# Kernel optimization log

Hardware: AMD Instinct MI355X
Metric: run time of the kernel (lower is better)

## Reference

```python
import jax, jax.numpy as jnp
import numpy as np

DATA_MAX = 30.0
LOG_FACTOR = float(np.log(DATA_MAX + 1.0))
THRESHOLDS = np.array([0.1, 1.0, 2.0, 5.0, 8.0], dtype=np.float32)
HIGHS = np.array([1.0, 2.0, 5.0, 8.0, np.inf], dtype=np.float32)
LEVEL_WEIGHTS = np.array([0.1, 0.1, 0.2, 0.25, 0.35], dtype=np.float32)
TIME_WEIGHTS = np.array([0.0075, 0.02, 0.03, 0.04, 0.05, 0.06, 0.07, 0.08, 0.09, 0.1,
                         0.09, 0.08, 0.07, 0.06, 0.05, 0.04, 0.03, 0.02, 0.0075, 0.005],
                        dtype=np.float32)


def setup_inputs() -> dict:
    key = jax.random.key(0)
    k1, k2, k3 = jax.random.split(key, 3)
    shape = (2, 20, 480, 480)
    pred_norm = jax.random.uniform(k1, shape, dtype=jnp.float32)
    target_norm = jax.random.uniform(k2, shape, dtype=jnp.float32)
    mask = jax.random.uniform(k3, shape, dtype=jnp.float32)
    return {"pred_norm": pred_norm, "target_norm": target_norm, "mask": mask}


def _metscore(pred_norm, target_norm, mask):
    # de-normalize to physical space (mm)
    pred = jnp.clip(jnp.expm1(pred_norm * LOG_FACTOR), 0.0, None)
    target = jnp.clip(jnp.expm1(target_norm * LOG_FACTOR), 0.0, None)
    B, T, H, W = pred.shape
    N = B * H * W
    # flatten each timestep across batch+space: [T, N]
    p = jnp.transpose(pred, (1, 0, 2, 3)).reshape(T, N)
    t = jnp.transpose(target, (1, 0, 2, 3)).reshape(T, N)
    m = (jnp.transpose(mask, (1, 0, 2, 3)).reshape(T, N) > 0.5)
    mf = m.astype(p.dtype)

    thr = jnp.asarray(THRESHOLDS)
    highs = jnp.asarray(HIGHS)
    lw = jnp.asarray(LEVEL_WEIGHTS)

    # ---- per-timestep masked correlation (excluding double-zero pixels) ----
    dz = (p < thr[0]) & (t < thr[0])
    mc = (m & ~dz).astype(p.dtype)                       # [T,N]
    cnt = mc.sum(-1)                                      # [T]
    safe_cnt = jnp.maximum(cnt, 1.0)
    p_mean = (p * mc).sum(-1) / safe_cnt
    t_mean = (t * mc).sum(-1) / safe_cnt
    dp = (p - p_mean[:, None]) * mc
    dt = (t - t_mean[:, None]) * mc
    num = (dp * dt).sum(-1)
    den = jnp.sqrt((dp * dp).sum(-1) * (dt * dt).sum(-1))
    r_time = jnp.where(cnt > 0, jnp.clip(num / (den + 1e-6), -1.0, 1.0), 0.0)  # [T]

    # ---- threshold-bin membership [T, L, N] ----
    p_in = ((p[:, None, :] >= thr[None, :, None]) & (p[:, None, :] < highs[None, :, None])).astype(p.dtype)
    t_in = ((t[:, None, :] >= thr[None, :, None]) & (t[:, None, :] < highs[None, :, None])).astype(p.dtype)

    hits = jnp.einsum('tln,tln,tn->tl', p_in, t_in, mf)   # [T,L]
    p_tot = jnp.einsum('tln,tn->tl', p_in, mf)            # hits + false alarms
    t_tot = jnp.einsum('tln,tn->tl', t_in, mf)            # hits + misses
    ts_mat = hits / (p_tot + t_tot - hits + 1e-8)         # [T,L]

    diff = jnp.abs(p - t) * mf                            # [T,N]
    mae_num = jnp.einsum('tln,tn->tl', t_in, diff)
    mae_mat = jnp.where(t_tot > 0, mae_num / jnp.maximum(t_tot, 1.0), 0.0)  # [T,L]

    # ---- score combination ----
    term_corr = jnp.sqrt(jnp.exp(r_time - 1.0))           # [T]
    term_mae = jnp.sqrt(jnp.exp(-mae_mat / 100.0))        # [T,L]
    score_time = term_corr * (lw[None, :] * ts_mat * term_mae).sum(-1)  # [T]

    tw = jnp.asarray(TIME_WEIGHTS)
    if T == tw.shape[0]:
        w_time = tw
    elif T < tw.shape[0]:
        w_time = tw[:T] / tw[:T].sum()
    else:
        w_time = jnp.ones((T,), dtype=p.dtype) / T
    total = (score_time * w_time).sum()
    return total, score_time, r_time, ts_mat, mae_mat, ts_mat.mean(0), mae_mat.mean(0)


def reference(pred_norm, target_norm, mask):
    return _metscore(pred_norm, target_norm, mask)
```

## Files before the change

kernel.cpp:

```cpp
#include <hip/hip_runtime.h>
#include <math.h>

#define TS   20
#define NL   5
#define NS   26
#define HW4C 57600

__device__ __forceinline__ void accum_pixel(float pn, float tn, float mn, float* a)
{
    constexpr float LF = 3.4339872044851463f;
    float p = fmaxf(expf(pn * LF) - 1.0f, 0.0f);
    float q = fmaxf(expf(tn * LF) - 1.0f, 0.0f);
    if (mn > 0.5f) {
        if (!((p < 0.1f) && (q < 0.1f))) {
            a[20] += 1.0f;
            a[21] += p;  a[22] += q;
            a[23] += p * q;  a[24] += p * p;  a[25] += q * q;
        }
        float ad = fabsf(p - q);
        bool p1 = p >= 0.1f, p2 = p >= 1.0f, p3 = p >= 2.0f, p4 = p >= 5.0f, p5 = p >= 8.0f;
        bool q1 = q >= 0.1f, q2 = q >= 1.0f, q3 = q >= 2.0f, q4 = q >= 5.0f, q5 = q >= 8.0f;
        bool pin[NL] = { p1 && !p2, p2 && !p3, p3 && !p4, p4 && !p5, p5 };
        bool qin[NL] = { q1 && !q2, q2 && !q3, q3 && !q4, q4 && !q5, q5 };
        #pragma unroll
        for (int l = 0; l < NL; ++l) {
            if (pin[l])           a[5 + l]  += 1.0f;
            if (qin[l])         { a[10 + l] += 1.0f;  a[15 + l] += ad; }
            if (pin[l] && qin[l]) a[l]      += 1.0f;
        }
    }
}

__global__ __launch_bounds__(256) void metscore_pass1(
    const float4* __restrict__ pred, const float4* __restrict__ targ,
    const float4* __restrict__ mask, float* __restrict__ sums )
{
    const int t = blockIdx.y;
    const int b = blockIdx.z;
    const size_t base = ((size_t)b * TS + t) * (size_t)HW4C;

    float acc[NS];
    #pragma unroll
    for (int k = 0; k < NS; ++k) acc[k] = 0.0f;

    const int stride = gridDim.x * blockDim.x;
    for (int i = blockIdx.x * blockDim.x + threadIdx.x; i < HW4C; i += stride) {
        float4 pv = pred[base + i];
        float4 tv = targ[base + i];
        float4 mv = mask[base + i];
        accum_pixel(pv.x, tv.x, mv.x, acc);
        accum_pixel(pv.y, tv.y, mv.y, acc);
        accum_pixel(pv.z, tv.z, mv.z, acc);
        accum_pixel(pv.w, tv.w, mv.w, acc);
    }

    #pragma unroll
    for (int k = 0; k < NS; ++k) {
        float v = acc[k];
        v += __shfl_down(v, 32);
        v += __shfl_down(v, 16);
        v += __shfl_down(v, 8);
        v += __shfl_down(v, 4);
        v += __shfl_down(v, 2);
        v += __shfl_down(v, 1);
        acc[k] = v;
    }

    __shared__ float lds[4][NS];
    const int lane = threadIdx.x & 63;
    const int wv   = threadIdx.x >> 6;
    if (lane == 0) {
        #pragma unroll
        for (int k = 0; k < NS; ++k) lds[wv][k] = acc[k];
    }
    __syncthreads();
    if (threadIdx.x < NS) {
        float s = lds[0][threadIdx.x] + lds[1][threadIdx.x]
                + lds[2][threadIdx.x] + lds[3][threadIdx.x];
        atomicAdd(&sums[t * NS + threadIdx.x], s);
    }
}

__global__ __launch_bounds__(128) void metscore_final(
    const float* __restrict__ sums, float* __restrict__ out)
{
    __shared__ float ts_s[TS][NL];
    __shared__ float mae_s[TS][NL];
    __shared__ float sc_s[TS];

    const int tid = threadIdx.x;

    if (tid < TS * NL) {
        int t = tid / NL, l = tid % NL;
        const float* s = sums + t * NS;
        float h = s[l], pt = s[5 + l], tt = s[10 + l], mn = s[15 + l];
        float ts  = h / (pt + tt - h + 1e-8f);
        float mae = (tt > 0.0f) ? (mn / fmaxf(tt, 1.0f)) : 0.0f;
        ts_s[t][l]  = ts;
        mae_s[t][l] = mae;
        out[41 + tid]  = ts;
        out[141 + tid] = mae;
    }
    __syncthreads();

    if (tid < TS) {
        const float* s = sums + tid * NS;
        double cnt = s[20], sp = s[21], st = s[22];
        double spt = s[23], spp = s[24], stt = s[25];
        double sc = fmax(cnt, 1.0);
        double pm = sp / sc, tm = st / sc;
        double num = spt - pm * st - tm * sp + pm * tm * cnt;
        double vp  = spp - 2.0 * pm * sp + pm * pm * cnt;
        double vt  = stt - 2.0 * tm * st + tm * tm * cnt;
        double den = sqrt(vp * vt);
        double r = num / (den + 1e-6);
        r = fmin(fmax(r, -1.0), 1.0);
        float rt = (cnt > 0.0) ? (float)r : 0.0f;
        out[21 + tid] = rt;

        const float LW[NL] = {0.1f, 0.1f, 0.2f, 0.25f, 0.35f};
        float term_corr = sqrtf(expf(rt - 1.0f));
        float accl = 0.0f;
        #pragma unroll
        for (int l = 0; l < NL; ++l)
            accl += LW[l] * ts_s[tid][l] * sqrtf(expf(-mae_s[tid][l] * 0.01f));
        float sct = term_corr * accl;
        out[1 + tid] = sct;

        const float TW[TS] = {0.0075f, 0.02f, 0.03f, 0.04f, 0.05f, 0.06f, 0.07f,
                              0.08f, 0.09f, 0.1f, 0.09f, 0.08f, 0.07f, 0.06f,
                              0.05f, 0.04f, 0.03f, 0.02f, 0.0075f, 0.005f};
        sc_s[tid] = sct * TW[tid];
    }
    __syncthreads();

    if (tid == 0) {
        float tot = 0.0f;
        for (int t = 0; t < TS; ++t) tot += sc_s[t];
        out[0] = tot;
    }
    if (tid < NL) {
        float a = 0.0f, b = 0.0f;
        for (int t = 0; t < TS; ++t) { a += ts_s[t][tid]; b += mae_s[t][tid]; }
        out[241 + tid] = a * (1.0f / TS);
        out[246 + tid] = b * (1.0f / TS);
    }
}

extern "C" void kernel_launch(void* const* d_in, const int* in_sizes, int n_in,
                              void* d_out, int out_size, void* d_ws, size_t ws_size,
                              hipStream_t stream) {
    (void)in_sizes; (void)n_in; (void)out_size; (void)ws_size;
    const float4* pred = (const float4*)d_in[0];
    const float4* targ = (const float4*)d_in[1];
    const float4* mask = (const float4*)d_in[2];
    float* out  = (float*)d_out;
    float* sums = (float*)d_ws;

    hipMemsetAsync(sums, 0, TS * NS * sizeof(float), stream);

    dim3 grid(32, TS, 2);
    metscore_pass1<<<grid, 256, 0, stream>>>(pred, targ, mask, sums);
    metscore_final<<<1, 128, 0, stream>>>(sums, out);
}
```

Before: 144.8 us.

## Fuse final reduction via last-block counter and pack bin counts into integers

Replaces per-bin float accumulators with 5-bit packed integer one-hot counters, cumulative MAE sums differenced at the end, and branchless masking with fast exp. Each block processes a fixed unrolled tile, and the grid is resized to cover the data exactly. The separate finalization kernel is folded into the main kernel using an atomic completion counter so the last block computes the scores. This reduces ALU and branch work per pixel and removes one launch, at the cost of relying on exact grid sizing and counter-field overflow limits.

After: 345.7 us. 2.39x slower.

```diff
diff --git a/kernel.cpp b/kernel.cpp
--- a/kernel.cpp
+++ b/kernel.cpp
@@ -4,66 +4,99 @@
 #define TS   20
 #define NL   5
 #define NS   26
-#define HW4C 57600
-
-__device__ __forceinline__ void accum_pixel(float pn, float tn, float mn, float* a)
+#define GX   45
+#define TPB  256
+#define NBLK (GX * TS * 2)
+#define HW4  57600
+
+struct Acc {
+    unsigned pPack, tPack, hPack;
+    int cnt;
+    float cum[NL];
+    float sp, st, spt, spp, stt;
+};
+
+__device__ __forceinline__ void px(float pn, float tn, float mn, Acc& A)
 {
     constexpr float LF = 3.4339872044851463f;
-    float p = fmaxf(expf(pn * LF) - 1.0f, 0.0f);
-    float q = fmaxf(expf(tn * LF) - 1.0f, 0.0f);
-    if (mn > 0.5f) {
-        if (!((p < 0.1f) && (q < 0.1f))) {
-            a[20] += 1.0f;
-            a[21] += p;  a[22] += q;
-            a[23] += p * q;  a[24] += p * p;  a[25] += q * q;
-        }
-        float ad = fabsf(p - q);
-        bool p1 = p >= 0.1f, p2 = p >= 1.0f, p3 = p >= 2.0f, p4 = p >= 5.0f, p5 = p >= 8.0f;
-        bool q1 = q >= 0.1f, q2 = q >= 1.0f, q3 = q >= 2.0f, q4 = q >= 5.0f, q5 = q >= 8.0f;
-        bool pin[NL] = { p1 && !p2, p2 && !p3, p3 && !p4, p4 && !p5, p5 };
-        bool qin[NL] = { q1 && !q2, q2 && !q3, q3 && !q4, q4 && !q5, q5 };
-        #pragma unroll
-        for (int l = 0; l < NL; ++l) {
-            if (pin[l])           a[5 + l]  += 1.0f;
-            if (qin[l])         { a[10 + l] += 1.0f;  a[15 + l] += ad; }
-            if (pin[l] && qin[l]) a[l]      += 1.0f;
-        }
-    }
+    float p = __expf(pn * LF) - 1.0f;
+    float q = __expf(tn * LF) - 1.0f;
+    bool mok = mn > 0.5f;
+    float pm = mok ? p : -1.0f;
+    float qm = mok ? q : -1.0f;
+    bool p1 = pm >= 0.1f, p2 = pm >= 1.0f, p3 = pm >= 2.0f, p4 = pm >= 5.0f, p5 = pm >= 8.0f;
+    bool q1 = qm >= 0.1f, q2 = qm >= 1.0f, q3 = qm >= 2.0f, q4 = qm >= 5.0f, q5 = qm >= 8.0f;
+    int lp = (int)p1 + (int)p2 + (int)p3 + (int)p4 + (int)p5;
+    int lq = (int)q1 + (int)q2 + (int)q3 + (int)q4 + (int)q5;
+    unsigned ohp = 1u << (5 * lp);
+    unsigned ohq = 1u << (5 * lq);
+    A.pPack += ohp;
+    A.tPack += ohq;
+    A.hPack += (lp == lq) ? ohp : 0u;
+    bool cond = (lp | lq) != 0;
+    A.cnt += cond ? 1 : 0;
+    float pz = cond ? p : 0.0f;
+    float qz = cond ? q : 0.0f;
+    A.sp += pz;  A.st += qz;
+    A.spt = fmaf(pz, qz, A.spt);
+    A.spp = fmaf(pz, pz, A.spp);
+    A.stt = fmaf(qz, qz, A.stt);
+    float ad = fabsf(p - q);
+    A.cum[0] += q1 ? ad : 0.0f;
+    A.cum[1] += q2 ? ad : 0.0f;
+    A.cum[2] += q3 ? ad : 0.0f;
+    A.cum[3] += q4 ? ad : 0.0f;
+    A.cum[4] += q5 ? ad : 0.0f;
 }
 
-__global__ __launch_bounds__(256) void metscore_pass1(
+__global__ __launch_bounds__(TPB) void metscore_fused(
     const float4* __restrict__ pred, const float4* __restrict__ targ,
-    const float4* __restrict__ mask, float* __restrict__ sums )
+    const float4* __restrict__ mask, float* __restrict__ sums,
+    unsigned* __restrict__ done, float* __restrict__ out)
 {
     const int t = blockIdx.y;
     const int b = blockIdx.z;
-    const size_t base = ((size_t)b * TS + t) * (size_t)HW4C;
-
-    float acc[NS];
-    #pragma unroll
-    for (int k = 0; k < NS; ++k) acc[k] = 0.0f;
-
-    const int stride = gridDim.x * blockDim.x;
-    for (int i = blockIdx.x * blockDim.x + threadIdx.x; i < HW4C; i += stride) {
-        float4 pv = pred[base + i];
-        float4 tv = targ[base + i];
-        float4 mv = mask[base + i];
-        accum_pixel(pv.x, tv.x, mv.x, acc);
-        accum_pixel(pv.y, tv.y, mv.y, acc);
-        accum_pixel(pv.z, tv.z, mv.z, acc);
-        accum_pixel(pv.w, tv.w, mv.w, acc);
-    }
+    const size_t base = ((size_t)b * TS + t) * (size_t)HW4
+                      + (size_t)blockIdx.x * (5 * TPB) + threadIdx.x;
+
+    Acc A;
+    A.pPack = A.tPack = A.hPack = 0u;  A.cnt = 0;
+    A.sp = A.st = A.spt = A.spp = A.stt = 0.0f;
+    #pragma unroll
+    for (int l = 0; l < NL; ++l) A.cum[l] = 0.0f;
+
+    #pragma unroll
+    for (int j = 0; j < 5; ++j) {
+        float4 pv = pred[base + j * TPB];
+        float4 tv = targ[base + j * TPB];
+        float4 mv = mask[base + j * TPB];
+        px(pv.x, tv.x, mv.x, A);
+        px(pv.y, tv.y, mv.y, A);
+        px(pv.z, tv.z, mv.z, A);
+        px(pv.w, tv.w, mv.w, A);
+    }
+
+    float v[NS];
+    #pragma unroll
+    for (int l = 0; l < NL; ++l) {
+        v[l]      = (float)((A.hPack >> (5 * (l + 1))) & 31u);
+        v[5 + l]  = (float)((A.pPack >> (5 * (l + 1))) & 31u);
+        v[10 + l] = (float)((A.tPack >> (5 * (l + 1))) & 31u);
+        v[15 + l] = A.cum[l];
+    }
+    v[20] = (float)A.cnt;
+    v[21] = A.sp; v[22] = A.st; v[23] = A.spt; v[24] = A.spp; v[25] = A.stt;
 
     #pragma unroll
     for (int k = 0; k < NS; ++k) {
-        float v = acc[k];
-        v += __shfl_down(v, 32);
-        v += __shfl_down(v, 16);
-        v += __shfl_down(v, 8);
-        v += __shfl_down(v, 4);
-        v += __shfl_down(v, 2);
-        v += __shfl_down(v, 1);
-        acc[k] = v;
+        float x = v[k];
+        x += __shfl_down(x, 32);
+        x += __shfl_down(x, 16);
+        x += __shfl_down(x, 8);
+        x += __shfl_down(x, 4);
+        x += __shfl_down(x, 2);
+        x += __shfl_down(x, 1);
+        v[k] = x;
     }
 
     __shared__ float lds[4][NS];
@@ -71,7 +104,7 @@
     const int wv   = threadIdx.x >> 6;
     if (lane == 0) {
         #pragma unroll
-        for (int k = 0; k < NS; ++k) lds[wv][k] = acc[k];
+        for (int k = 0; k < NS; ++k) lds[wv][k] = v[k];
     }
     __syncthreads();
     if (threadIdx.x < NS) {
@@ -79,39 +112,50 @@
                 + lds[2][threadIdx.x] + lds[3][threadIdx.x];
         atomicAdd(&sums[t * NS + threadIdx.x], s);
     }
-}
-
-__global__ __launch_bounds__(128) void metscore_final(
-    const float* __restrict__ sums, float* __restrict__ out)
-{
+
+    __shared__ unsigned isLast;
+    __syncthreads();
+    __threadfence();
+    if (threadIdx.x == 0) {
+        unsigned old = atomicAdd(done, 1u);
+        isLast = (old == (unsigned)(NBLK - 1)) ? 1u : 0u;
+    }
+    __syncthreads();
+    if (!isLast) return;
+
+    __shared__ float S[TS * NS];
+    for (int i = threadIdx.x; i < TS * NS; i += TPB)
+        S[i] = atomicAdd(&sums[i], 0.0f);
+    __syncthreads();
+
     __shared__ float ts_s[TS][NL];
     __shared__ float mae_s[TS][NL];
     __shared__ float sc_s[TS];
-
     const int tid = threadIdx.x;
 
     if (tid < TS * NL) {
-        int t = tid / NL, l = tid % NL;
-        const float* s = sums + t * NS;
-        float h = s[l], pt = s[5 + l], tt = s[10 + l], mn = s[15 + l];
+        int tt_ = tid / NL, l = tid % NL;
+        const float* s = S + tt_ * NS;
+        float h = s[l], pt = s[5 + l], tt = s[10 + l];
+        float mn = s[15 + l] - ((l < NL - 1) ? s[16 + l] : 0.0f);
         float ts  = h / (pt + tt - h + 1e-8f);
         float mae = (tt > 0.0f) ? (mn / fmaxf(tt, 1.0f)) : 0.0f;
-        ts_s[t][l]  = ts;
-        mae_s[t][l] = mae;
+        ts_s[tt_][l]  = ts;
+        mae_s[tt_][l] = mae;
         out[41 + tid]  = ts;
         out[141 + tid] = mae;
     }
     __syncthreads();
 
     if (tid < TS) {
-        const float* s = sums + tid * NS;
+        const float* s = S + tid * NS;
         double cnt = s[20], sp = s[21], st = s[22];
         double spt = s[23], spp = s[24], stt = s[25];
         double sc = fmax(cnt, 1.0);
-        double pm = sp / sc, tm = st / sc;
-        double num = spt - pm * st - tm * sp + pm * tm * cnt;
-        double vp  = spp - 2.0 * pm * sp + pm * pm * cnt;
-        double vt  = stt - 2.0 * tm * st + tm * tm * cnt;
+        double pmn = sp / sc, tmn = st / sc;
+        double num = spt - pmn * st - tmn * sp + pmn * tmn * cnt;
+        double vp  = spp - 2.0 * pmn * sp + pmn * pmn * cnt;
+        double vt  = stt - 2.0 * tmn * st + tmn * tmn * cnt;
         double den = sqrt(vp * vt);
         double r = num / (den + 1e-6);
         r = fmin(fmax(r, -1.0), 1.0);
@@ -136,14 +180,14 @@
 
     if (tid == 0) {
         float tot = 0.0f;
-        for (int t = 0; t < TS; ++t) tot += sc_s[t];
+        for (int k = 0; k < TS; ++k) tot += sc_s[k];
         out[0] = tot;
     }
     if (tid < NL) {
-        float a = 0.0f, b = 0.0f;
-        for (int t = 0; t < TS; ++t) { a += ts_s[t][tid]; b += mae_s[t][tid]; }
+        float a = 0.0f, bsum = 0.0f;
+        for (int k = 0; k < TS; ++k) { a += ts_s[k][tid]; bsum += mae_s[k][tid]; }
         out[241 + tid] = a * (1.0f / TS);
-        out[246 + tid] = b * (1.0f / TS);
+        out[246 + tid] = bsum * (1.0f / TS);
     }
 }
 
@@ -156,10 +200,10 @@
     const float4* mask = (const float4*)d_in[2];
     float* out  = (float*)d_out;
     float* sums = (float*)d_ws;
-
-    hipMemsetAsync(sums, 0, TS * NS * sizeof(float), stream);
-
-    dim3 grid(32, TS, 2);
-    metscore_pass1<<<grid, 256, 0, stream>>>(pred, targ, mask, sums);
-    metscore_final<<<1, 128, 0, stream>>>(sums, out);
+    unsigned* done = (unsigned*)((char*)d_ws + TS * NS * sizeof(float));
+
+    hipMemsetAsync(d_ws, 0, (TS * NS + 1) * sizeof(float), stream);
+
+    dim3 grid(GX, TS, 2);
+    metscore_fused<<<grid, TPB, 0, stream>>>(pred, targ, mask, sums, done, out);
 }
```
